# Kernel optimization log

Measured on AMD Instinct MI355X. Metric: run time of the kernel, lower is better.

The kernel has to match this reference:

```python
import jax, jax.numpy as jnp
import numpy as np
from itertools import permutations

B, Nm, S, K, H, OUT = 32, 128, 16, 4, 128, 1
LG, LI, LGL = 3, 2, 2  # num_layer, num_layer_id, num_layer_global
EPS = 1e-5


def _ln(x, g, b):
    m = jnp.mean(x, -1, keepdims=True)
    v = jnp.mean(jnp.square(x - m), -1, keepdims=True)
    return (x - m) * jax.lax.rsqrt(v + EPS) * g + b


def _block(x, W1, b1, W2, b2, g, bn):
    # Linear -> ReLU -> Linear -> LayerNorm -> ReLU
    h = jax.nn.relu(x @ W1 + b1)
    return jax.nn.relu(_ln(h @ W2 + b2, g, bn))


def setup_inputs() -> dict:
    key = jax.random.key(0)
    ks = iter(jax.random.split(key, 64))
    nrm = lambda shape, s=0.05: jax.random.normal(next(ks), shape, jnp.float32) * s
    x = nrm((B, Nm, 1), 1.0)
    adj = (jax.random.uniform(next(ks), (B, Nm, Nm)) < 0.05).astype(jnp.float32)
    # allperm: all permutations of [1..K-1] with 0 prepended, transposed -> (K, permdim)
    ap = np.array(list(permutations(range(1, K))), dtype=np.int32)
    ap = np.concatenate([np.zeros((ap.shape[0], 1), np.int32), ap], axis=1).T
    allperm = jnp.asarray(ap)
    Ssub = B * S
    base = jax.random.randint(next(ks), (Ssub,), 0, Nm - K)
    subgs = base[:, None] + jnp.arange(K, dtype=jnp.int32)[None, :]  # distinct nodes per subgraph
    num_subg = jnp.full((B,), S, jnp.int32)
    num_node = jnp.full((B,), Nm, jnp.int32)
    d = dict(x=x, adj=adj,
             idemb=nrm((K + 2, H)),
             in_W1=nrm((1, H)), in_b1=jnp.zeros((H,)), in_W2=nrm((H, H)), in_b2=jnp.zeros((H,)),
             in_g=jnp.ones((H,)), in_bn=jnp.zeros((H,)),
             gW1=nrm((LG, H, H)), gb1=jnp.zeros((LG, H)), gW2=nrm((LG, H, H)), gb2=jnp.zeros((LG, H)),
             gg=jnp.ones((LG, H)), gbn=jnp.zeros((LG, H)),
             iW1=nrm((LI, H, H)), ib1=jnp.zeros((LI, H)), iW2=nrm((LI, H, H)), ib2=jnp.zeros((LI, H)),
             ig=jnp.ones((LI, H)), ibn=jnp.zeros((LI, H)),
             glW1=nrm((LGL, H, H)), glb1=jnp.zeros((LGL, H)), glW2=nrm((LGL, H, H)), glb2=jnp.zeros((LGL, H)),
             glg=jnp.ones((LGL, H)), glbn=jnp.zeros((LGL, H)),
             s1_W=nrm((H, H)), s1_b=jnp.zeros((H,)), s2_W=nrm((H, H)), s2_b=jnp.zeros((H,)),
             rW1=nrm((H, H)), rb1=jnp.zeros((H,)), rW2=nrm((H, H)), rb2=jnp.zeros((H,)),
             rg=jnp.ones((H,)), rbn=jnp.zeros((H,)),
             out_W=nrm((H, OUT)), out_b=jnp.zeros((OUT,)),
             subgs=subgs, num_subg=num_subg, num_node=num_node, allperm=allperm)
    return d


def reference(x, adj, idemb, in_W1, in_b1, in_W2, in_b2, in_g, in_bn,
              gW1, gb1, gW2, gb2, gg, gbn,
              iW1, ib1, iW2, ib2, ig, ibn,
              glW1, glb1, glW2, glb2, glg, glbn,
              s1_W, s1_b, s2_W, s2_b,
              rW1, rb1, rW2, rb2, rg, rbn,
              out_W, out_b, subgs, num_subg, num_node, allperm):
    Bsz, N = x.shape[0], x.shape[1]
    Ssub, k = subgs.shape
    permdim = allperm.shape[1]
    # input embedding MLP
    h = _block(x, in_W1, in_b1, in_W2, in_b2, in_g, in_bn)  # (B, Nm, H)
    Hd = h.shape[-1]
    # subgraph -> graph batch map (ns_b = S per graph; Ssub static)
    subgbatch = jnp.repeat(jnp.arange(Bsz), num_subg, total_repeat_length=Ssub)
    # identity labeling: z starts as ones, labeled nodes get idemb(allperm[pos])
    lb = jnp.repeat(jnp.arange(Ssub), k)          # label batch (subgraph idx)
    lnodes = subgs.reshape(-1)                    # node ids within graph
    ni = jnp.tile(jnp.arange(k), Ssub)            # position within subgraph
    vals = idemb[allperm[ni]]                     # (Ssub*k, permdim, H)
    z = jnp.ones((Ssub, N, permdim, Hd), x.dtype)
    z = z.at[lb, lnodes].multiply(vals)
    # graph message passing on full graphs
    for l in range(gW1.shape[0]):
        m = jnp.einsum('bij,bjd->bid', adj, h)
        h = h + _block(m, gW1[l], gb1[l], gW2[l], gb2[l], gg[l], gbn[l])
    hs = h[subgbatch]        # (Ssub, Nm, H)
    sadj = adj[subgbatch]    # (Ssub, Nm, Nm)
    # id message passing over permutation channels
    for l in range(iW1.shape[0]):
        m = jnp.einsum('bij,bjpd->bipd', sadj, z)
        z = z + _block(m, iW1[l], ib1[l], iW2[l], ib2[l], ig[l], ibn[l])
    # zero out padded (null) nodes
    null_mask = jnp.arange(N)[None, :] >= num_node[:, None]  # (B, Nm)
    z = jnp.where(null_mask[subgbatch][:, :, None, None], 0.0, z)
    z = jax.nn.relu(z.mean(axis=2) @ s1_W + s1_b)  # setmlp1, (Ssub, Nm, H)
    hs = hs + z
    for l in range(glW1.shape[0]):
        m = jnp.einsum('bij,bjd->bid', sadj, hs)
        hs = hs + _block(m, glW1[l], glb1[l], glW2[l], glb2[l], glg[l], glbn[l])
    hs = jax.nn.relu(hs.sum(axis=1) @ s2_W + s2_b)  # setmlp2, (Ssub, H)
    pooled = jax.ops.segment_max(hs, subgbatch, num_segments=Bsz)  # global max pool
    pooled = pooled + _block(pooled, rW1, rb1, rW2, rb2, rg, rbn)  # setmlp3 (1 layer)
    return pooled @ out_W + out_b  # (B, OUT)
```

## Files before the change

kernel.cpp:

```cpp
#include <hip/hip_runtime.h>
#include <hip/hip_bf16.h>
#include <string.h>

typedef __hip_bfloat16 bf16;
typedef short v8s __attribute__((ext_vector_type(8)));
typedef float v4f __attribute__((ext_vector_type(4)));

#define H_ 128
#define P_ 6
#define K_ 4

__device__ __forceinline__ float ldf(const float* p, size_t i) { return p[i]; }
__device__ __forceinline__ float ldf(const bf16* p, size_t i) { return __bfloat162float(p[i]); }

__device__ __forceinline__ float s2f(short s) {
    unsigned int u = ((unsigned int)(unsigned short)s) << 16;
    float f; __builtin_memcpy(&f, &u, 4); return f;
}
__device__ __forceinline__ short f2s(float v) {
    bf16 h = __float2bfloat16(v);
    short s; __builtin_memcpy(&s, &h, 2); return s;
}
__device__ __forceinline__ v4f MFMA(v8s a, v8s b, v4f c) {
    return __builtin_amdgcn_mfma_f32_16x16x32_bf16(a, b, c, 0, 0, 0);
}

__global__ __launch_bounds__(128) void k_deg(const float* __restrict__ adj, float* __restrict__ degf)
{
    __shared__ float red[128];
    const int row = blockIdx.x, t = threadIdx.x;
    red[t] = adj[(size_t)row * 128 + t];
    __syncthreads();
    for (int s = 64; s > 0; s >>= 1) {
        if (t < s) red[t] += red[t + s];
        __syncthreads();
    }
    if (t == 0) degf[row] = red[0];
}

__global__ __launch_bounds__(128) void k_adjb(const float* __restrict__ adj, bf16* __restrict__ adjb)
{
    const size_t i = (size_t)blockIdx.x * 128 + threadIdx.x;
    adjb[i] = __float2bfloat16(adj[i]);
}

__global__ __launch_bounds__(128) void k_wt8(
    const float* s0, const float* s1, const float* s2, const float* s3,
    const float* s4, const float* s5, const float* s6, const float* s7,
    bf16* __restrict__ dst)
{
    const int w = blockIdx.x >> 7, n = blockIdx.x & 127, k = threadIdx.x;
    const float* arr[8] = {s0, s1, s2, s3, s4, s5, s6, s7};
    dst[(size_t)w * 16384 + n * 128 + k] = __float2bfloat16(arr[w][k * 128 + n]);
}

__global__ __launch_bounds__(128) void k_wt1(const float* __restrict__ src, bf16* __restrict__ dst)
{
    const int n = blockIdx.x, k = threadIdx.x;
    dst[n * 128 + k] = __float2bfloat16(src[k * 128 + n]);
}

template<bool DO_MM1, bool HAS_RES>
__global__ __launch_bounds__(128) void k_block(
    const float* __restrict__ in, const float* __restrict__ res, float* __restrict__ out,
    const float* __restrict__ W1, const float* __restrict__ b1,
    const float* __restrict__ W2, const float* __restrict__ b2,
    const float* __restrict__ gam, const float* __restrict__ bet)
{
    __shared__ float sA[16][136];
    __shared__ float sB[16][136];
    __shared__ float sStat[32];
    const int hd = threadIdx.x;
    const size_t row0 = (size_t)blockIdx.x * 16;
    #pragma unroll
    for (int r = 0; r < 16; ++r) sA[r][hd] = in[(row0 + r) * H_ + hd];
    __syncthreads();
    float acc[16];
    if (DO_MM1) {
        #pragma unroll
        for (int r = 0; r < 16; ++r) acc[r] = b1[hd];
        for (int k = 0; k < H_; k += 4) {
            float w0 = W1[(k+0)*H_+hd], w1 = W1[(k+1)*H_+hd], w2 = W1[(k+2)*H_+hd], w3 = W1[(k+3)*H_+hd];
            #pragma unroll
            for (int r = 0; r < 16; ++r) {
                float4 a = *(const float4*)&sA[r][k];
                acc[r] = fmaf(a.x, w0, acc[r]); acc[r] = fmaf(a.y, w1, acc[r]);
                acc[r] = fmaf(a.z, w2, acc[r]); acc[r] = fmaf(a.w, w3, acc[r]);
            }
        }
        #pragma unroll
        for (int r = 0; r < 16; ++r) sB[r][hd] = fmaxf(acc[r], 0.f);
    } else {
        #pragma unroll
        for (int r = 0; r < 16; ++r) sB[r][hd] = sA[r][hd];
    }
    __syncthreads();
    #pragma unroll
    for (int r = 0; r < 16; ++r) acc[r] = b2[hd];
    for (int k = 0; k < H_; k += 4) {
        float w0 = W2[(k+0)*H_+hd], w1 = W2[(k+1)*H_+hd], w2 = W2[(k+2)*H_+hd], w3 = W2[(k+3)*H_+hd];
        #pragma unroll
        for (int r = 0; r < 16; ++r) {
            float4 a = *(const float4*)&sB[r][k];
            acc[r] = fmaf(a.x, w0, acc[r]); acc[r] = fmaf(a.y, w1, acc[r]);
            acc[r] = fmaf(a.z, w2, acc[r]); acc[r] = fmaf(a.w, w3, acc[r]);
        }
    }
    __syncthreads();
    #pragma unroll
    for (int r = 0; r < 16; ++r) sA[r][hd] = acc[r];
    __syncthreads();
    if (hd < 16) {
        float s = 0.f, ss = 0.f;
        for (int k = 0; k < H_; ++k) { float v = sA[hd][k]; s += v; ss += v * v; }
        float mean = s * (1.f / H_);
        float var = ss * (1.f / H_) - mean * mean;
        sStat[hd] = mean; sStat[16 + hd] = rsqrtf(var + 1e-5f);
    }
    __syncthreads();
    float gv = gam[hd], bv = bet[hd];
    #pragma unroll
    for (int r = 0; r < 16; ++r) {
        float v = fmaxf((acc[r] - sStat[r]) * sStat[16 + r] * gv + bv, 0.f);
        if (HAS_RES) v += res[(row0 + r) * H_ + hd];
        out[(row0 + r) * H_ + hd] = v;
    }
}

template<bool GATHER, typename T>
__global__ __launch_bounds__(128) void k_gemm_relu(
    const T* __restrict__ in, const float* __restrict__ res, float* __restrict__ out,
    const float* __restrict__ W, const float* __restrict__ b)
{
    __shared__ float sA[16][136];
    const int hd = threadIdx.x;
    const size_t row0 = (size_t)blockIdx.x * 16;
    #pragma unroll
    for (int r = 0; r < 16; ++r) sA[r][hd] = ldf(in, (row0 + r) * H_ + hd);
    __syncthreads();
    float acc[16];
    #pragma unroll
    for (int r = 0; r < 16; ++r) acc[r] = b[hd];
    for (int k = 0; k < H_; k += 4) {
        float w0 = W[(k+0)*H_+hd], w1 = W[(k+1)*H_+hd], w2 = W[(k+2)*H_+hd], w3 = W[(k+3)*H_+hd];
        #pragma unroll
        for (int r = 0; r < 16; ++r) {
            float4 a = *(const float4*)&sA[r][k];
            acc[r] = fmaf(a.x, w0, acc[r]); acc[r] = fmaf(a.y, w1, acc[r]);
            acc[r] = fmaf(a.z, w2, acc[r]); acc[r] = fmaf(a.w, w3, acc[r]);
        }
    }
    #pragma unroll
    for (int r = 0; r < 16; ++r) {
        size_t rr = row0 + r;
        float v = fmaxf(acc[r], 0.f);
        if (GATHER) {
            int i = (int)(rr & 127);
            int g = (int)(rr >> 11);
            v += res[((size_t)(g * 128 + i)) * H_ + hd];
        }
        out[rr * H_ + hd] = v;
    }
}

__global__ __launch_bounds__(256) void k_h_fused(
    const float* __restrict__ x, const bf16* __restrict__ adjb,
    const float* __restrict__ inW1, const float* __restrict__ inb1,
    const bf16* __restrict__ inW2t, const float* __restrict__ inb2,
    const float* __restrict__ ing, const float* __restrict__ inbn,
    const bf16* __restrict__ WTg,
    const float* __restrict__ gb1, const float* __restrict__ gb2,
    const float* __restrict__ gg, const float* __restrict__ gbn,
    float* __restrict__ hb)
{
    __shared__ __align__(16) short sHsT[128][136];
    __shared__ __align__(16) short sM[128][136];
    __shared__ float sP[15][128];
    const int t = threadIdx.x;
    const int g = blockIdx.x;
    const int wave = t >> 6, lane = t & 63, quad = lane >> 4, l16 = lane & 15;
    const int wrow = wave << 5;

    for (int u = t; u < 15 * 128; u += 256) {
        const int a = u >> 7, n = u & 127;
        const float* src;
        if (a == 0) src = inb2;
        else if (a == 1) src = ing;
        else if (a == 2) src = inbn;
        else {
            const int l = (a - 3) >> 2, pp = (a - 3) & 3;
            src = (pp == 0) ? gb1 + l * 128 : (pp == 1) ? gb2 + l * 128
                : (pp == 2) ? gg + l * 128 : gbn + l * 128;
        }
        sP[a][n] = src[n];
    }

    v8s aA[2][4];
    {
        const bf16* ar = adjb + (size_t)g * 16384;
        #pragma unroll
        for (int mt = 0; mt < 2; ++mt)
            #pragma unroll
            for (int kk = 0; kk < 4; ++kk)
                aA[mt][kk] = *(const v8s*)(ar + (size_t)(wrow + mt * 16 + l16) * 128 + kk * 32 + quad * 8);
    }

    {
        const int i = t >> 1, half = (t & 1) * 64;
        const float xv = x[(size_t)g * 128 + i];
        #pragma unroll
        for (int fb = 0; fb < 64; fb += 8) {
            v8s pk;
            #pragma unroll
            for (int e = 0; e < 8; ++e)
                pk[e] = f2s(fmaxf(fmaf(xv, inW1[half + fb + e], inb1[half + fb + e]), 0.f));
            *(v8s*)&sM[i][half + fb] = pk;
        }
    }
    __syncthreads();

    v4f acc[2][8];
    #pragma unroll
    for (int mt = 0; mt < 2; ++mt)
        #pragma unroll
        for (int nt = 0; nt < 8; ++nt) acc[mt][nt] = (v4f){0.f, 0.f, 0.f, 0.f};
    #pragma unroll
    for (int kk = 0; kk < 4; ++kk) {
        v8s a0 = *(const v8s*)&sM[wrow + l16][kk * 32 + quad * 8];
        v8s a1 = *(const v8s*)&sM[wrow + 16 + l16][kk * 32 + quad * 8];
        #pragma unroll
        for (int nt = 0; nt < 8; ++nt) {
            v8s b = *(const v8s*)(inW2t + (nt * 16 + l16) * 128 + kk * 32 + quad * 8);
            acc[0][nt] = MFMA(a0, b, acc[0][nt]);
            acc[1][nt] = MFMA(a1, b, acc[1][nt]);
        }
    }
    float hs_reg[2][8][4];
    #pragma unroll
    for (int mt = 0; mt < 2; ++mt)
        #pragma unroll
        for (int r = 0; r < 4; ++r) {
            float s = 0.f, qq = 0.f;
            #pragma unroll
            for (int nt = 0; nt < 8; ++nt) {
                float u = acc[mt][nt][r] + sP[0][nt * 16 + l16];
                acc[mt][nt][r] = u;
                s += u; qq += u * u;
            }
            #pragma unroll
            for (int d = 1; d < 16; d <<= 1) {
                s += __shfl_xor(s, d);
                qq += __shfl_xor(qq, d);
            }
            float mn = s * (1.f / 128.f);
            float rs = rsqrtf(qq * (1.f / 128.f) - mn * mn + 1e-5f);
            const int i = wrow + mt * 16 + quad * 4 + r;
            #pragma unroll
            for (int nt = 0; nt < 8; ++nt) {
                const int n = nt * 16 + l16;
                float v = fmaxf((acc[mt][nt][r] - mn) * rs * sP[1][n] + sP[2][n], 0.f);
                hs_reg[mt][nt][r] = v;
                sHsT[n][i] = f2s(v);
            }
        }
    __syncthreads();

    for (int l = 0; l < 3; ++l) {
        const bf16* W1t = WTg + (size_t)(2 * l) * 16384;
        const bf16* W2t = WTg + (size_t)(2 * l + 1) * 16384;
        #pragma unroll
        for (int mt = 0; mt < 2; ++mt)
            #pragma unroll
            for (int nt = 0; nt < 8; ++nt) acc[mt][nt] = (v4f){0.f, 0.f, 0.f, 0.f};
        #pragma unroll
        for (int kk = 0; kk < 4; ++kk)
            #pragma unroll
            for (int nt = 0; nt < 8; ++nt) {
                v8s b = *(const v8s*)&sHsT[nt * 16 + l16][kk * 32 + quad * 8];
                acc[0][nt] = MFMA(aA[0][kk], b, acc[0][nt]);
                acc[1][nt] = MFMA(aA[1][kk], b, acc[1][nt]);
            }
        #pragma unroll
        for (int nt = 0; nt < 8; ++nt)
            #pragma unroll
            for (int mt = 0; mt < 2; ++mt)
                #pragma unroll
                for (int r = 0; r < 4; ++r)
                    sM[wrow + mt * 16 + quad * 4 + r][nt * 16 + l16] = f2s(acc[mt][nt][r]);
        __syncthreads();
        #pragma unroll
        for (int mt = 0; mt < 2; ++mt)
            #pragma unroll
            for (int nt = 0; nt < 8; ++nt) acc[mt][nt] = (v4f){0.f, 0.f, 0.f, 0.f};
        #pragma unroll
        for (int kk = 0; kk < 4; ++kk) {
            v8s a0 = *(const v8s*)&sM[wrow + l16][kk * 32 + quad * 8];
            v8s a1 = *(const v8s*)&sM[wrow + 16 + l16][kk * 32 + quad * 8];
            #pragma unroll
            for (int nt = 0; nt < 8; ++nt) {
                v8s b = *(const v8s*)(W1t + (nt * 16 + l16) * 128 + kk * 32 + quad * 8);
                acc[0][nt] = MFMA(a0, b, acc[0][nt]);
                acc[1][nt] = MFMA(a1, b, acc[1][nt]);
            }
        }
        #pragma unroll
        for (int nt = 0; nt < 8; ++nt) {
            float bb = sP[3 + 4 * l + 0][nt * 16 + l16];
            #pragma unroll
            for (int mt = 0; mt < 2; ++mt)
                #pragma unroll
                for (int r = 0; r < 4; ++r)
                    sM[wrow + mt * 16 + quad * 4 + r][nt * 16 + l16] = f2s(fmaxf(acc[mt][nt][r] + bb, 0.f));
        }
        #pragma unroll
        for (int mt = 0; mt < 2; ++mt)
            #pragma unroll
            for (int nt = 0; nt < 8; ++nt) acc[mt][nt] = (v4f){0.f, 0.f, 0.f, 0.f};
        #pragma unroll
        for (int kk = 0; kk < 4; ++kk) {
            v8s a0 = *(const v8s*)&sM[wrow + l16][kk * 32 + quad * 8];
            v8s a1 = *(const v8s*)&sM[wrow + 16 + l16][kk * 32 + quad * 8];
            #pragma unroll
            for (int nt = 0; nt < 8; ++nt) {
                v8s b = *(const v8s*)(W2t + (nt * 16 + l16) * 128 + kk * 32 + quad * 8);
                acc[0][nt] = MFMA(a0, b, acc[0][nt]);
                acc[1][nt] = MFMA(a1, b, acc[1][nt]);
            }
        }
        #pragma unroll
        for (int mt = 0; mt < 2; ++mt)
            #pragma unroll
            for (int r = 0; r < 4; ++r) {
                float s = 0.f, qq = 0.f;
                #pragma unroll
                for (int nt = 0; nt < 8; ++nt) {
                    float u = acc[mt][nt][r] + sP[3 + 4 * l + 1][nt * 16 + l16];
                    acc[mt][nt][r] = u;
                    s += u; qq += u * u;
                }
                #pragma unroll
                for (int d = 1; d < 16; d <<= 1) {
                    s += __shfl_xor(s, d);
                    qq += __shfl_xor(qq, d);
                }
                float mn = s * (1.f / 128.f);
                float rs = rsqrtf(qq * (1.f / 128.f) - mn * mn + 1e-5f);
                const int i = wrow + mt * 16 + quad * 4 + r;
                #pragma unroll
                for (int nt = 0; nt < 8; ++nt) {
                    const int n = nt * 16 + l16;
                    float v = fmaxf((acc[mt][nt][r] - mn) * rs * sP[3 + 4 * l + 2][n] + sP[3 + 4 * l + 3][n], 0.f);
                    float h2 = hs_reg[mt][nt][r] + v;
                    hs_reg[mt][nt][r] = h2;
                    sHsT[n][i] = f2s(h2);
                }
            }
        __syncthreads();
    }

    #pragma unroll
    for (int mt = 0; mt < 2; ++mt)
        #pragma unroll
        for (int nt = 0; nt < 8; ++nt)
            #pragma unroll
            for (int r = 0; r < 4; ++r) {
                const int i = wrow + mt * 16 + quad * 4 + r;
                const int n = nt * 16 + l16;
                hb[((size_t)(g * 128 + i)) * 128 + n] = hs_reg[mt][nt][r];
            }
}

__global__ __launch_bounds__(256) void k_id1_fused(
    const float* __restrict__ adj, const float* __restrict__ degf,
    const int* __restrict__ subgs, const int* __restrict__ allperm,
    const float* __restrict__ idemb, bf16* __restrict__ outb,
    const bf16* __restrict__ W1t, const float* __restrict__ b1,
    const bf16* __restrict__ W2t, const float* __restrict__ b2,
    const float* __restrict__ gam, const float* __restrict__ bet)
{
    __shared__ __align__(16) short sB[128][136];
    __shared__ float sE[K_][128];
    const int t = threadIdx.x;
    const int bi = blockIdx.x;
    const int b_s = bi / 6, p = bi - b_s * 6;
    const int g = b_s >> 4;
    const int wave = t >> 6, lane = t & 63;
    const int quad = lane >> 4, l16 = lane & 15;
    const int wrow = wave << 5;

    int nodeq[K_];
    #pragma unroll
    for (int q = 0; q < K_; ++q) nodeq[q] = subgs[b_s * K_ + q];

    for (int u = t; u < K_ * 128; u += 256) {
        const int q = u >> 7, f = u & 127;
        sE[q][f] = idemb[(size_t)allperm[q * P_ + p] * H_ + f] - 1.f;
    }
    __syncthreads();

    {
        const int i = t >> 1, half = (t & 1) * 64;
        const int gi = g * 128 + i;
        const float dg = degf[gi];
        float aq[K_];
        #pragma unroll
        for (int q = 0; q < K_; ++q) aq[q] = adj[(size_t)gi * 128 + nodeq[q]];
        #pragma unroll
        for (int f = 0; f < 64; ++f) {
            float v = dg;
            #pragma unroll
            for (int q = 0; q < K_; ++q) v = fmaf(aq[q], sE[q][half + f], v);
            sB[i][half + f] = f2s(v);
        }
    }
    __syncthreads();

    v4f acc[2][8];
    #pragma unroll
    for (int mt = 0; mt < 2; ++mt)
        #pragma unroll
        for (int nt = 0; nt < 8; ++nt) acc[mt][nt] = (v4f){0.f, 0.f, 0.f, 0.f};
    #pragma unroll
    for (int kk = 0; kk < 4; ++kk) {
        v8s a0 = *(const v8s*)&sB[wrow + l16][kk * 32 + quad * 8];
        v8s a1 = *(const v8s*)&sB[wrow + 16 + l16][kk * 32 + quad * 8];
        #pragma unroll
        for (int nt = 0; nt < 8; ++nt) {
            v8s b = *(const v8s*)(W1t + (nt * 16 + l16) * 128 + kk * 32 + quad * 8);
            acc[0][nt] = MFMA(a0, b, acc[0][nt]);
            acc[1][nt] = MFMA(a1, b, acc[1][nt]);
        }
    }
    #pragma unroll
    for (int nt = 0; nt < 8; ++nt) {
        float bb = b1[nt * 16 + l16];
        #pragma unroll
        for (int mt = 0; mt < 2; ++mt)
            #pragma unroll
            for (int r = 0; r < 4; ++r)
                sB[wrow + mt * 16 + quad * 4 + r][nt * 16 + l16] = f2s(fmaxf(acc[mt][nt][r] + bb, 0.f));
    }
    #pragma unroll
    for (int mt = 0; mt < 2; ++mt)
        #pragma unroll
        for (int nt = 0; nt < 8; ++nt) acc[mt][nt] = (v4f){0.f, 0.f, 0.f, 0.f};
    #pragma unroll
    for (int kk = 0; kk < 4; ++kk) {
        v8s a0 = *(const v8s*)&sB[wrow + l16][kk * 32 + quad * 8];
        v8s a1 = *(const v8s*)&sB[wrow + 16 + l16][kk * 32 + quad * 8];
        #pragma unroll
        for (int nt = 0; nt < 8; ++nt) {
            v8s b = *(const v8s*)(W2t + (nt * 16 + l16) * 128 + kk * 32 + quad * 8);
            acc[0][nt] = MFMA(a0, b, acc[0][nt]);
            acc[1][nt] = MFMA(a1, b, acc[1][nt]);
        }
    }
    float bb2[8], gv[8], bv[8];
    #pragma unroll
    for (int nt = 0; nt < 8; ++nt) {
        int n = nt * 16 + l16;
        bb2[nt] = b2[n]; gv[nt] = gam[n]; bv[nt] = bet[n];
    }
    #pragma unroll
    for (int mt = 0; mt < 2; ++mt)
        #pragma unroll
        for (int r = 0; r < 4; ++r) {
            float s = 0.f, q = 0.f;
            #pragma unroll
            for (int nt = 0; nt < 8; ++nt) {
                float u = acc[mt][nt][r] + bb2[nt];
                acc[mt][nt][r] = u;
                s += u; q += u * u;
            }
            #pragma unroll
            for (int d = 1; d < 16; d <<= 1) {
                s += __shfl_xor(s, d);
                q += __shfl_xor(q, d);
            }
            float mn = s * (1.f / 128.f);
            float rs = rsqrtf(q * (1.f / 128.f) - mn * mn + 1e-5f);
            #pragma unroll
            for (int nt = 0; nt < 8; ++nt) {
                float v = fmaxf((acc[mt][nt][r] - mn) * rs * gv[nt] + bv[nt], 0.f);
                sB[wrow + mt * 16 + quad * 4 + r][nt * 16 + l16] = f2s(v + 1.0f);
            }
        }
    __syncthreads();
    {
        const int f = t >> 1, nh = (t & 1) * 64;
        const short* flat = &sB[0][0];
        bf16* dst = outb + (size_t)bi * 16384 + (size_t)f * 128 + nh;
        #pragma unroll
        for (int u = 0; u < 8; ++u) {
            v8s pk;
            #pragma unroll
            for (int e = 0; e < 8; ++e) pk[e] = flat[(nh + u * 8 + e) * 136 + f];
            *(v8s*)(dst + u * 8) = pk;
        }
    }
}

__global__ __launch_bounds__(256) void k_id2_v9(
    const bf16* __restrict__ z2t, bf16* __restrict__ zm,
    const bf16* __restrict__ adjb, const int* __restrict__ num_node,
    const int* __restrict__ subgs, const int* __restrict__ allperm,
    const float* __restrict__ idemb,
    const bf16* __restrict__ W1t, const float* __restrict__ b1,
    const bf16* __restrict__ W2t, const float* __restrict__ b2,
    const float* __restrict__ gam, const float* __restrict__ bet)
{
    __shared__ __align__(16) short sB[128][136];
    __shared__ float sP[4][128];
    const int t = threadIdx.x;
    const int b_s = blockIdx.x;
    const int g = b_s >> 4;
    const int wave = t >> 6, lane = t & 63, quad = lane >> 4, l16 = lane & 15;
    const int wrow = wave << 5;

    #pragma unroll
    for (int u = 0; u < 2; ++u) {
        const int v = t + u * 256;
        const int a = v >> 7, n = v & 127;
        const float* src = (a == 0) ? b1 : (a == 1) ? b2 : (a == 2) ? gam : bet;
        sP[a][n] = src[n];
    }

    v8s aA[2][4];
    {
        const bf16* ar = adjb + (size_t)g * 16384;
        #pragma unroll
        for (int mt = 0; mt < 2; ++mt)
            #pragma unroll
            for (int kk = 0; kk < 4; ++kk)
                aA[mt][kk] = *(const v8s*)(ar + (size_t)(wrow + mt * 16 + l16) * 128 + kk * 32 + quad * 8);
    }
    int nodeq[K_];
    #pragma unroll
    for (int q = 0; q < K_; ++q) nodeq[q] = subgs[b_s * K_ + q];

    float macc[2][8][4];
    #pragma unroll
    for (int mt = 0; mt < 2; ++mt)
        #pragma unroll
        for (int nt = 0; nt < 8; ++nt)
            #pragma unroll
            for (int r = 0; r < 4; ++r) macc[mt][nt][r] = 0.f;

    const int sf = t >> 1, shalf = (t & 1) * 64;

    for (int p = 0; p < P_; ++p) {
        {
            const bf16* src = z2t + ((size_t)(b_s * P_ + p)) * 16384 + (size_t)sf * 128 + shalf;
            #pragma unroll
            for (int u = 0; u < 8; ++u)
                *(v8s*)&sB[sf][shalf + u * 8] = *(const v8s*)(src + u * 8);
        }
        __syncthreads();
        if (t < 128) {
            #pragma unroll
            for (int q = 0; q < K_; ++q) {
                float e = idemb[(size_t)allperm[q * P_ + p] * H_ + t] - 1.f;
                short* cell = &sB[t][nodeq[q]];
                *cell = f2s(s2f(*cell) + e);
            }
        }
        __syncthreads();
        #pragma unroll
        for (int mt = 0; mt < 2; ++mt)
            #pragma unroll
            for (int nt = 0; nt < 8; ++nt) {
                const int n = nt * 16 + l16;
                #pragma unroll
                for (int r = 0; r < 4; ++r)
                    macc[mt][nt][r] += s2f(sB[n][wrow + mt * 16 + quad * 4 + r]);
            }
        v4f acc[2][8];
        #pragma unroll
        for (int mt = 0; mt < 2; ++mt)
            #pragma unroll
            for (int nt = 0; nt < 8; ++nt) acc[mt][nt] = (v4f){0.f, 0.f, 0.f, 0.f};
        #pragma unroll
        for (int kk = 0; kk < 4; ++kk)
            #pragma unroll
            for (int nt = 0; nt < 8; ++nt) {
                v8s b = *(const v8s*)&sB[nt * 16 + l16][kk * 32 + quad * 8];
                acc[0][nt] = MFMA(aA[0][kk], b, acc[0][nt]);
                acc[1][nt] = MFMA(aA[1][kk], b, acc[1][nt]);
            }
        __syncthreads();
        #pragma unroll
        for (int nt = 0; nt < 8; ++nt)
            #pragma unroll
            for (int mt = 0; mt < 2; ++mt)
                #pragma unroll
                for (int r = 0; r < 4; ++r)
                    sB[wrow + mt * 16 + quad * 4 + r][nt * 16 + l16] = f2s(acc[mt][nt][r]);
        #pragma unroll
        for (int mt = 0; mt < 2; ++mt)
            #pragma unroll
            for (int nt = 0; nt < 8; ++nt) acc[mt][nt] = (v4f){0.f, 0.f, 0.f, 0.f};
        #pragma unroll
        for (int kk = 0; kk < 4; ++kk) {
            v8s a0 = *(const v8s*)&sB[wrow + l16][kk * 32 + quad * 8];
            v8s a1 = *(const v8s*)&sB[wrow + 16 + l16][kk * 32 + quad * 8];
            #pragma unroll
            for (int nt = 0; nt < 8; ++nt) {
                v8s b = *(const v8s*)(W1t + (nt * 16 + l16) * 128 + kk * 32 + quad * 8);
                acc[0][nt] = MFMA(a0, b, acc[0][nt]);
                acc[1][nt] = MFMA(a1, b, acc[1][nt]);
            }
        }
        #pragma unroll
        for (int nt = 0; nt < 8; ++nt) {
            float bb = sP[0][nt * 16 + l16];
            #pragma unroll
            for (int mt = 0; mt < 2; ++mt)
                #pragma unroll
                for (int r = 0; r < 4; ++r)
                    sB[wrow + mt * 16 + quad * 4 + r][nt * 16 + l16] = f2s(fmaxf(acc[mt][nt][r] + bb, 0.f));
        }
        #pragma unroll
        for (int mt = 0; mt < 2; ++mt)
            #pragma unroll
            for (int nt = 0; nt < 8; ++nt) acc[mt][nt] = (v4f){0.f, 0.f, 0.f, 0.f};
        #pragma unroll
        for (int kk = 0; kk < 4; ++kk) {
            v8s a0 = *(const v8s*)&sB[wrow + l16][kk * 32 + quad * 8];
            v8s a1 = *(const v8s*)&sB[wrow + 16 + l16][kk * 32 + quad * 8];
            #pragma unroll
            for (int nt = 0; nt < 8; ++nt) {
                v8s b = *(const v8s*)(W2t + (nt * 16 + l16) * 128 + kk * 32 + quad * 8);
                acc[0][nt] = MFMA(a0, b, acc[0][nt]);
                acc[1][nt] = MFMA(a1, b, acc[1][nt]);
            }
        }
        #pragma unroll
        for (int mt = 0; mt < 2; ++mt)
            #pragma unroll
            for (int r = 0; r < 4; ++r) {
                float s = 0.f, qq = 0.f;
                #pragma unroll
                for (int nt = 0; nt < 8; ++nt) {
                    float u = acc[mt][nt][r] + sP[1][nt * 16 + l16];
                    acc[mt][nt][r] = u;
                    s += u; qq += u * u;
                }
                #pragma unroll
                for (int d = 1; d < 16; d <<= 1) {
                    s += __shfl_xor(s, d);
                    qq += __shfl_xor(qq, d);
                }
                float mn = s * (1.f / 128.f);
                float rs = rsqrtf(qq * (1.f / 128.f) - mn * mn + 1e-5f);
                #pragma unroll
                for (int nt = 0; nt < 8; ++nt) {
                    const int n = nt * 16 + l16;
                    macc[mt][nt][r] += fmaxf((acc[mt][nt][r] - mn) * rs * sP[2][n] + sP[3][n], 0.f);
                }
            }
        __syncthreads();
    }
    const int nn = num_node[g];
    #pragma unroll
    for (int mt = 0; mt < 2; ++mt)
        #pragma unroll
        for (int nt = 0; nt < 8; ++nt)
            #pragma unroll
            for (int r = 0; r < 4; ++r) {
                const int i = wrow + mt * 16 + quad * 4 + r;
                const int n = nt * 16 + l16;
                float v = (i >= nn) ? 0.f : macc[mt][nt][r] * (1.f / 6.f);
                zm[((size_t)(b_s * 128 + i)) * 128 + n] = __float2bfloat16(v);
            }
}

__global__ __launch_bounds__(256) void k_gl_fused(
    const bf16* __restrict__ zm, const float* __restrict__ hb,
    const bf16* __restrict__ adjb,
    const bf16* __restrict__ s1Wt, const float* __restrict__ s1_b,
    const bf16* __restrict__ WTgl,
    const float* __restrict__ glb1, const float* __restrict__ glb2,
    const float* __restrict__ glg, const float* __restrict__ glbn,
    float* __restrict__ hsum)
{
    __shared__ __align__(16) short sHsT[128][136];
    __shared__ __align__(16) short sM[128][136];
    __shared__ float sP[9][128];
    const int t = threadIdx.x;
    const int b_s = blockIdx.x;
    const int g = b_s >> 4;
    const int wave = t >> 6, lane = t & 63, quad = lane >> 4, l16 = lane & 15;
    const int wrow = wave << 5;

    for (int u = t; u < 9 * 128; u += 256) {
        const int a = u >> 7, n = u & 127;
        const float* src =
            (a == 0) ? glb1 : (a == 1) ? glb2 : (a == 2) ? glg : (a == 3) ? glbn :
            (a == 4) ? glb1 + 128 : (a == 5) ? glb2 + 128 : (a == 6) ? glg + 128 :
            (a == 7) ? glbn + 128 : s1_b;
        sP[a][n] = src[n];
    }

    v8s aA[2][4];
    {
        const bf16* ar = adjb + (size_t)g * 16384;
        #pragma unroll
        for (int mt = 0; mt < 2; ++mt)
            #pragma unroll
            for (int kk = 0; kk < 4; ++kk)
                aA[mt][kk] = *(const v8s*)(ar + (size_t)(wrow + mt * 16 + l16) * 128 + kk * 32 + quad * 8);
    }

    v4f acc[2][8];
    #pragma unroll
    for (int mt = 0; mt < 2; ++mt)
        #pragma unroll
        for (int nt = 0; nt < 8; ++nt) acc[mt][nt] = (v4f){0.f, 0.f, 0.f, 0.f};
    #pragma unroll
    for (int kk = 0; kk < 4; ++kk) {
        v8s a0 = *(const v8s*)(zm + ((size_t)(b_s * 128) + wrow + l16) * 128 + kk * 32 + quad * 8);
        v8s a1 = *(const v8s*)(zm + ((size_t)(b_s * 128) + wrow + 16 + l16) * 128 + kk * 32 + quad * 8);
        #pragma unroll
        for (int nt = 0; nt < 8; ++nt) {
            v8s b = *(const v8s*)(s1Wt + (nt * 16 + l16) * 128 + kk * 32 + quad * 8);
            acc[0][nt] = MFMA(a0, b, acc[0][nt]);
            acc[1][nt] = MFMA(a1, b, acc[1][nt]);
        }
    }
    __syncthreads();
    float hs_reg[2][8][4];
    #pragma unroll
    for (int mt = 0; mt < 2; ++mt)
        #pragma unroll
        for (int nt = 0; nt < 8; ++nt)
            #pragma unroll
            for (int r = 0; r < 4; ++r) {
                const int i = wrow + mt * 16 + quad * 4 + r;
                const int n = nt * 16 + l16;
                float v = fmaxf(acc[mt][nt][r] + sP[8][n], 0.f);
                v += hb[((size_t)(g * 128 + i)) * 128 + n];
                hs_reg[mt][nt][r] = v;
                sHsT[n][i] = f2s(v);
            }
    __syncthreads();

    for (int l = 0; l < 2; ++l) {
        const bf16* W1t = WTgl + (size_t)(2 * l) * 16384;
        const bf16* W2t = WTgl + (size_t)(2 * l + 1) * 16384;
        #pragma unroll
        for (int mt = 0; mt < 2; ++mt)
            #pragma unroll
            for (int nt = 0; nt < 8; ++nt) acc[mt][nt] = (v4f){0.f, 0.f, 0.f, 0.f};
        #pragma unroll
        for (int kk = 0; kk < 4; ++kk)
            #pragma unroll
            for (int nt = 0; nt < 8; ++nt) {
                v8s b = *(const v8s*)&sHsT[nt * 16 + l16][kk * 32 + quad * 8];
                acc[0][nt] = MFMA(aA[0][kk], b, acc[0][nt]);
                acc[1][nt] = MFMA(aA[1][kk], b, acc[1][nt]);
            }
        #pragma unroll
        for (int nt = 0; nt < 8; ++nt)
            #pragma unroll
            for (int mt = 0; mt < 2; ++mt)
                #pragma unroll
                for (int r = 0; r < 4; ++r)
                    sM[wrow + mt * 16 + quad * 4 + r][nt * 16 + l16] = f2s(acc[mt][nt][r]);
        __syncthreads();
        #pragma unroll
        for (int mt = 0; mt < 2; ++mt)
            #pragma unroll
            for (int nt = 0; nt < 8; ++nt) acc[mt][nt] = (v4f){0.f, 0.f, 0.f, 0.f};
        #pragma unroll
        for (int kk = 0; kk < 4; ++kk) {
            v8s a0 = *(const v8s*)&sM[wrow + l16][kk * 32 + quad * 8];
            v8s a1 = *(const v8s*)&sM[wrow + 16 + l16][kk * 32 + quad * 8];
            #pragma unroll
            for (int nt = 0; nt < 8; ++nt) {
                v8s b = *(const v8s*)(W1t + (nt * 16 + l16) * 128 + kk * 32 + quad * 8);
                acc[0][nt] = MFMA(a0, b, acc[0][nt]);
                acc[1][nt] = MFMA(a1, b, acc[1][nt]);
            }
        }
        #pragma unroll
        for (int nt = 0; nt < 8; ++nt) {
            float bb = sP[4 * l + 0][nt * 16 + l16];
            #pragma unroll
            for (int mt = 0; mt < 2; ++mt)
                #pragma unroll
                for (int r = 0; r < 4; ++r)
                    sM[wrow + mt * 16 + quad * 4 + r][nt * 16 + l16] = f2s(fmaxf(acc[mt][nt][r] + bb, 0.f));
        }
        #pragma unroll
        for (int mt = 0; mt < 2; ++mt)
            #pragma unroll
            for (int nt = 0; nt < 8; ++nt) acc[mt][nt] = (v4f){0.f, 0.f, 0.f, 0.f};
        #pragma unroll
        for (int kk = 0; kk < 4; ++kk) {
            v8s a0 = *(const v8s*)&sM[wrow + l16][kk * 32 + quad * 8];
            v8s a1 = *(const v8s*)&sM[wrow + 16 + l16][kk * 32 + quad * 8];
            #pragma unroll
            for (int nt = 0; nt < 8; ++nt) {
                v8s b = *(const v8s*)(W2t + (nt * 16 + l16) * 128 + kk * 32 + quad * 8);
                acc[0][nt] = MFMA(a0, b, acc[0][nt]);
                acc[1][nt] = MFMA(a1, b, acc[1][nt]);
            }
        }
        #pragma unroll
        for (int mt = 0; mt < 2; ++mt)
            #pragma unroll
            for (int r = 0; r < 4; ++r) {
                float s = 0.f, qq = 0.f;
                #pragma unroll
                for (int nt = 0; nt < 8; ++nt) {
                    float u = acc[mt][nt][r] + sP[4 * l + 1][nt * 16 + l16];
                    acc[mt][nt][r] = u;
                    s += u; qq += u * u;
                }
                #pragma unroll
                for (int d = 1; d < 16; d <<= 1) {
                    s += __shfl_xor(s, d);
                    qq += __shfl_xor(qq, d);
                }
                float mn = s * (1.f / 128.f);
                float rs = rsqrtf(qq * (1.f / 128.f) - mn * mn + 1e-5f);
                const int i = wrow + mt * 16 + quad * 4 + r;
                #pragma unroll
                for (int nt = 0; nt < 8; ++nt) {
                    const int n = nt * 16 + l16;
                    float v = fmaxf((acc[mt][nt][r] - mn) * rs * sP[4 * l + 2][n] + sP[4 * l + 3][n], 0.f);
                    float h2 = hs_reg[mt][nt][r] + v;
                    hs_reg[mt][nt][r] = h2;
                    sHsT[n][i] = f2s(h2);
                }
            }
        __syncthreads();
    }

    float* sRedf = (float*)&sM[0][0];
    #pragma unroll
    for (int nt = 0; nt < 8; ++nt) {
        float part = 0.f;
        #pragma unroll
        for (int mt = 0; mt < 2; ++mt)
            #pragma unroll
            for (int r = 0; r < 4; ++r) part += hs_reg[mt][nt][r];
        sRedf[(wave * 4 + quad) * 128 + nt * 16 + l16] = part;
    }
    __syncthreads();
    if (t < 128) {
        float s = 0.f;
        #pragma unroll
        for (int r = 0; r < 16; ++r) s += sRedf[r * 128 + t];
        hsum[(size_t)b_s * 128 + t] = s;
    }
}

__global__ __launch_bounds__(128) void k_maxpool(const float* __restrict__ hs2, float* __restrict__ pooled)
{
    const int g = blockIdx.x, hd = threadIdx.x;
    float m = -INFINITY;
    for (int s = 0; s < 16; ++s) m = fmaxf(m, hs2[((size_t)(g * 16 + s)) * H_ + hd]);
    pooled[(size_t)g * H_ + hd] = m;
}

__global__ __launch_bounds__(128) void k_out(const float* __restrict__ pooled2,
    const float* __restrict__ out_W, const float* __restrict__ out_b, float* __restrict__ out)
{
    __shared__ float red[128];
    const int g = blockIdx.x, hd = threadIdx.x;
    red[hd] = pooled2[(size_t)g * H_ + hd] * out_W[hd];
    __syncthreads();
    for (int s = 64; s > 0; s >>= 1) {
        if (hd < s) red[hd] += red[hd + s];
        __syncthreads();
    }
    if (hd == 0) out[g] = red[0] + out_b[0];
}

extern "C" void kernel_launch(void* const* d_in, const int* in_sizes, int n_in,
                              void* d_out, int out_size, void* d_ws, size_t ws_size,
                              hipStream_t stream)
{
    (void)in_sizes; (void)n_in; (void)out_size; (void)ws_size;
    const float* x     = (const float*)d_in[0];
    const float* adj   = (const float*)d_in[1];
    const float* idemb = (const float*)d_in[2];
    const float* in_W1 = (const float*)d_in[3];
    const float* in_b1 = (const float*)d_in[4];
    const float* in_W2 = (const float*)d_in[5];
    const float* in_b2 = (const float*)d_in[6];
    const float* in_g  = (const float*)d_in[7];
    const float* in_bn = (const float*)d_in[8];
    const float* gW1   = (const float*)d_in[9];
    const float* gb1   = (const float*)d_in[10];
    const float* gW2   = (const float*)d_in[11];
    const float* gb2   = (const float*)d_in[12];
    const float* gg    = (const float*)d_in[13];
    const float* gbn   = (const float*)d_in[14];
    const float* iW1   = (const float*)d_in[15];
    const float* ib1   = (const float*)d_in[16];
    const float* iW2   = (const float*)d_in[17];
    const float* ib2   = (const float*)d_in[18];
    const float* ig    = (const float*)d_in[19];
    const float* ibn   = (const float*)d_in[20];
    const float* glW1  = (const float*)d_in[21];
    const float* glb1  = (const float*)d_in[22];
    const float* glW2  = (const float*)d_in[23];
    const float* glb2  = (const float*)d_in[24];
    const float* glg   = (const float*)d_in[25];
    const float* glbn  = (const float*)d_in[26];
    const float* s1_W  = (const float*)d_in[27];
    const float* s1_b  = (const float*)d_in[28];
    const float* s2_W  = (const float*)d_in[29];
    const float* s2_b  = (const float*)d_in[30];
    const float* rW1   = (const float*)d_in[31];
    const float* rb1   = (const float*)d_in[32];
    const float* rW2   = (const float*)d_in[33];
    const float* rb2   = (const float*)d_in[34];
    const float* rg    = (const float*)d_in[35];
    const float* rbn   = (const float*)d_in[36];
    const float* out_W = (const float*)d_in[37];
    const float* out_b = (const float*)d_in[38];
    const int* subgs   = (const int*)d_in[39];
    const int* num_node= (const int*)d_in[41];
    const int* allperm = (const int*)d_in[42];

    const size_t MB_ = (size_t)512 * 128 * P_ * H_ * 2;
    char* w = (char*)d_ws;
    bf16*  mz     = (bf16*)(w);
    bf16*  s1Wt   = (bf16*)(w + 33554432ull);
    bf16*  zm     = (bf16*)(w + MB_);
    bf16*  WT     = (bf16*)(w + MB_ + 16777216ull);
    char*  wc     = w + MB_ + 16777216ull + 262144ull;
    float* hb     = (float*)(wc);
    bf16*  adjb   = (bf16*)(wc + 2097152ull);
    bf16*  WT2    = (bf16*)(wc + 3145728ull);
    float* hsum   = (float*)(wc + 4194304ull);
    float* hs2    = (float*)(wc + 4456448ull);
    float* pooled = (float*)(wc + 4718592ull);
    float* pooled2= (float*)(wc + 4734976ull);
    float* degf   = (float*)(wc + 4964352ull);
    float* outp   = (float*)d_out;

    k_deg<<<4096, 128, 0, stream>>>(adj, degf);
    k_wt8<<<1024, 128, 0, stream>>>(iW1, iW2, iW1 + 16384, iW2 + 16384,
                                    glW1, glW2, glW1 + 16384, glW2 + 16384, WT);
    k_wt8<<<1024, 128, 0, stream>>>(in_W2, gW1, gW2, gW1 + 16384,
                                    gW2 + 16384, gW1 + 32768, gW2 + 32768, in_W2, WT2);
    k_adjb<<<4096, 128, 0, stream>>>(adj, adjb);

    k_h_fused<<<32, 256, 0, stream>>>(x, adjb, in_W1, in_b1,
        WT2, in_b2, in_g, in_bn,
        WT2 + 16384, gb1, gb2, gg, gbn, hb);

    k_id1_fused<<<3072, 256, 0, stream>>>(adj, degf, subgs, allperm, idemb, mz,
        WT, ib1, WT + 16384, ib2, ig, ibn);

    k_id2_v9<<<512, 256, 0, stream>>>(mz, zm, adjb, num_node, subgs, allperm, idemb,
        WT + 2 * 16384, ib1 + 128, WT + 3 * 16384, ib2 + 128, ig + 128, ibn + 128);

    k_wt1<<<128, 128, 0, stream>>>(s1_W, s1Wt);

    k_gl_fused<<<512, 256, 0, stream>>>(zm, hb, adjb, s1Wt, s1_b,
        WT + 4 * 16384, glb1, glb2, glg, glbn, hsum);

    k_gemm_relu<false, float><<<32, 128, 0, stream>>>(hsum, nullptr, hs2, s2_W, s2_b);
    k_maxpool<<<32, 128, 0, stream>>>(hs2, pooled);
    k_block<true, true><<<2, 128, 0, stream>>>(pooled, pooled, pooled2,
        rW1, rb1, rW2, rb2, rg, rbn);
    k_out<<<32, 128, 0, stream>>>(pooled2, out_W, out_b, outp);
}
```

Before: 589.8 us.

## Fuse tail kernels into one and share a single LDS buffer in gl kernel

Replaces the separate s2 gemm, max-pool, readout block and output-dot kernels with a single per-graph tail kernel, removing three launches and intermediate global buffers. In the gl fused kernel, the transposed-hs and message LDS buffers are merged into one, with extra barriers added so the buffer can be safely reused. This roughly halves LDS use, which can allow more resident blocks, at the cost of extra synchronisation.

```diff
diff --git a/kernel.cpp b/kernel.cpp
--- a/kernel.cpp
+++ b/kernel.cpp
@@ -9,9 +9,6 @@
 #define H_ 128
 #define P_ 6
 #define K_ 4
-
-__device__ __forceinline__ float ldf(const float* p, size_t i) { return p[i]; }
-__device__ __forceinline__ float ldf(const bf16* p, size_t i) { return __bfloat162float(p[i]); }
 
 __device__ __forceinline__ float s2f(short s) {
     unsigned int u = ((unsigned int)(unsigned short)s) << 16;
@@ -58,109 +55,6 @@
 {
     const int n = blockIdx.x, k = threadIdx.x;
     dst[n * 128 + k] = __float2bfloat16(src[k * 128 + n]);
-}
-
-template<bool DO_MM1, bool HAS_RES>
-__global__ __launch_bounds__(128) void k_block(
-    const float* __restrict__ in, const float* __restrict__ res, float* __restrict__ out,
-    const float* __restrict__ W1, const float* __restrict__ b1,
-    const float* __restrict__ W2, const float* __restrict__ b2,
-    const float* __restrict__ gam, const float* __restrict__ bet)
-{
-    __shared__ float sA[16][136];
-    __shared__ float sB[16][136];
-    __shared__ float sStat[32];
-    const int hd = threadIdx.x;
-    const size_t row0 = (size_t)blockIdx.x * 16;
-    #pragma unroll
-    for (int r = 0; r < 16; ++r) sA[r][hd] = in[(row0 + r) * H_ + hd];
-    __syncthreads();
-    float acc[16];
-    if (DO_MM1) {
-        #pragma unroll
-        for (int r = 0; r < 16; ++r) acc[r] = b1[hd];
-        for (int k = 0; k < H_; k += 4) {
-            float w0 = W1[(k+0)*H_+hd], w1 = W1[(k+1)*H_+hd], w2 = W1[(k+2)*H_+hd], w3 = W1[(k+3)*H_+hd];
-            #pragma unroll
-            for (int r = 0; r < 16; ++r) {
-                float4 a = *(const float4*)&sA[r][k];
-                acc[r] = fmaf(a.x, w0, acc[r]); acc[r] = fmaf(a.y, w1, acc[r]);
-                acc[r] = fmaf(a.z, w2, acc[r]); acc[r] = fmaf(a.w, w3, acc[r]);
-            }
-        }
-        #pragma unroll
-        for (int r = 0; r < 16; ++r) sB[r][hd] = fmaxf(acc[r], 0.f);
-    } else {
-        #pragma unroll
-        for (int r = 0; r < 16; ++r) sB[r][hd] = sA[r][hd];
-    }
-    __syncthreads();
-    #pragma unroll
-    for (int r = 0; r < 16; ++r) acc[r] = b2[hd];
-    for (int k = 0; k < H_; k += 4) {
-        float w0 = W2[(k+0)*H_+hd], w1 = W2[(k+1)*H_+hd], w2 = W2[(k+2)*H_+hd], w3 = W2[(k+3)*H_+hd];
-        #pragma unroll
-        for (int r = 0; r < 16; ++r) {
-            float4 a = *(const float4*)&sB[r][k];
-            acc[r] = fmaf(a.x, w0, acc[r]); acc[r] = fmaf(a.y, w1, acc[r]);
-            acc[r] = fmaf(a.z, w2, acc[r]); acc[r] = fmaf(a.w, w3, acc[r]);
-        }
-    }
-    __syncthreads();
-    #pragma unroll
-    for (int r = 0; r < 16; ++r) sA[r][hd] = acc[r];
-    __syncthreads();
-    if (hd < 16) {
-        float s = 0.f, ss = 0.f;
-        for (int k = 0; k < H_; ++k) { float v = sA[hd][k]; s += v; ss += v * v; }
-        float mean = s * (1.f / H_);
-        float var = ss * (1.f / H_) - mean * mean;
-        sStat[hd] = mean; sStat[16 + hd] = rsqrtf(var + 1e-5f);
-    }
-    __syncthreads();
-    float gv = gam[hd], bv = bet[hd];
-    #pragma unroll
-    for (int r = 0; r < 16; ++r) {
-        float v = fmaxf((acc[r] - sStat[r]) * sStat[16 + r] * gv + bv, 0.f);
-        if (HAS_RES) v += res[(row0 + r) * H_ + hd];
-        out[(row0 + r) * H_ + hd] = v;
-    }
-}
-
-template<bool GATHER, typename T>
-__global__ __launch_bounds__(128) void k_gemm_relu(
-    const T* __restrict__ in, const float* __restrict__ res, float* __restrict__ out,
-    const float* __restrict__ W, const float* __restrict__ b)
-{
-    __shared__ float sA[16][136];
-    const int hd = threadIdx.x;
-    const size_t row0 = (size_t)blockIdx.x * 16;
-    #pragma unroll
-    for (int r = 0; r < 16; ++r) sA[r][hd] = ldf(in, (row0 + r) * H_ + hd);
-    __syncthreads();
-    float acc[16];
-    #pragma unroll
-    for (int r = 0; r < 16; ++r) acc[r] = b[hd];
-    for (int k = 0; k < H_; k += 4) {
-        float w0 = W[(k+0)*H_+hd], w1 = W[(k+1)*H_+hd], w2 = W[(k+2)*H_+hd], w3 = W[(k+3)*H_+hd];
-        #pragma unroll
-        for (int r = 0; r < 16; ++r) {
-            float4 a = *(const float4*)&sA[r][k];
-            acc[r] = fmaf(a.x, w0, acc[r]); acc[r] = fmaf(a.y, w1, acc[r]);
-            acc[r] = fmaf(a.z, w2, acc[r]); acc[r] = fmaf(a.w, w3, acc[r]);
-        }
-    }
-    #pragma unroll
-    for (int r = 0; r < 16; ++r) {
-        size_t rr = row0 + r;
-        float v = fmaxf(acc[r], 0.f);
-        if (GATHER) {
-            int i = (int)(rr & 127);
-            int g = (int)(rr >> 11);
-            v += res[((size_t)(g * 128 + i)) * H_ + hd];
-        }
-        out[rr * H_ + hd] = v;
-    }
 }
 
 __global__ __launch_bounds__(256) void k_h_fused(
@@ -683,8 +577,7 @@
     const float* __restrict__ glg, const float* __restrict__ glbn,
     float* __restrict__ hsum)
 {
-    __shared__ __align__(16) short sHsT[128][136];
-    __shared__ __align__(16) short sM[128][136];
+    __shared__ __align__(16) short sB[128][136];
     __shared__ float sP[9][128];
     const int t = threadIdx.x;
     const int b_s = blockIdx.x;
@@ -740,7 +633,7 @@
                 float v = fmaxf(acc[mt][nt][r] + sP[8][n], 0.f);
                 v += hb[((size_t)(g * 128 + i)) * 128 + n];
                 hs_reg[mt][nt][r] = v;
-                sHsT[n][i] = f2s(v);
+                sB[n][i] = f2s(v);
             }
     __syncthreads();
 
@@ -755,26 +648,26 @@
         for (int kk = 0; kk < 4; ++kk)
             #pragma unroll
             for (int nt = 0; nt < 8; ++nt) {
-                v8s b = *(const v8s*)&sHsT[nt * 16 + l16][kk * 32 + quad * 8];
+                v8s b = *(const v8s*)&sB[nt * 16 + l16][kk * 32 + quad * 8];
                 acc[0][nt] = MFMA(aA[0][kk], b, acc[0][nt]);
                 acc[1][nt] = MFMA(aA[1][kk], b, acc[1][nt]);
             }
+        __syncthreads();
         #pragma unroll
         for (int nt = 0; nt < 8; ++nt)
             #pragma unroll
             for (int mt = 0; mt < 2; ++mt)
                 #pragma unroll
                 for (int r = 0; r < 4; ++r)
-                    sM[wrow + mt * 16 + quad * 4 + r][nt * 16 + l16] = f2s(acc[mt][nt][r]);
-        __syncthreads();
+                    sB[wrow + mt * 16 + quad * 4 + r][nt * 16 + l16] = f2s(acc[mt][nt][r]);
         #pragma unroll
         for (int mt = 0; mt < 2; ++mt)
             #pragma unroll
             for (int nt = 0; nt < 8; ++nt) acc[mt][nt] = (v4f){0.f, 0.f, 0.f, 0.f};
         #pragma unroll
         for (int kk = 0; kk < 4; ++kk) {
-            v8s a0 = *(const v8s*)&sM[wrow + l16][kk * 32 + quad * 8];
-            v8s a1 = *(const v8s*)&sM[wrow + 16 + l16][kk * 32 + quad * 8];
+            v8s a0 = *(const v8s*)&sB[wrow + l16][kk * 32 + quad * 8];
+            v8s a1 = *(const v8s*)&sB[wrow + 16 + l16][kk * 32 + quad * 8];
             #pragma unroll
             for (int nt = 0; nt < 8; ++nt) {
                 v8s b = *(const v8s*)(W1t + (nt * 16 + l16) * 128 + kk * 32 + quad * 8);
@@ -789,7 +682,7 @@
             for (int mt = 0; mt < 2; ++mt)
                 #pragma unroll
                 for (int r = 0; r < 4; ++r)
-                    sM[wrow + mt * 16 + quad * 4 + r][nt * 16 + l16] = f2s(fmaxf(acc[mt][nt][r] + bb, 0.f));
+                    sB[wrow + mt * 16 + quad * 4 + r][nt * 16 + l16] = f2s(fmaxf(acc[mt][nt][r] + bb, 0.f));
         }
         #pragma unroll
         for (int mt = 0; mt < 2; ++mt)
@@ -797,8 +690,8 @@
             for (int nt = 0; nt < 8; ++nt) acc[mt][nt] = (v4f){0.f, 0.f, 0.f, 0.f};
         #pragma unroll
         for (int kk = 0; kk < 4; ++kk) {
-            v8s a0 = *(const v8s*)&sM[wrow + l16][kk * 32 + quad * 8];
-            v8s a1 = *(const v8s*)&sM[wrow + 16 + l16][kk * 32 + quad * 8];
+            v8s a0 = *(const v8s*)&sB[wrow + l16][kk * 32 + quad * 8];
+            v8s a1 = *(const v8s*)&sB[wrow + 16 + l16][kk * 32 + quad * 8];
             #pragma unroll
             for (int nt = 0; nt < 8; ++nt) {
                 v8s b = *(const v8s*)(W2t + (nt * 16 + l16) * 128 + kk * 32 + quad * 8);
@@ -806,6 +699,7 @@
                 acc[1][nt] = MFMA(a1, b, acc[1][nt]);
             }
         }
+        __syncthreads();
         #pragma unroll
         for (int mt = 0; mt < 2; ++mt)
             #pragma unroll
@@ -831,13 +725,13 @@
                     float v = fmaxf((acc[mt][nt][r] - mn) * rs * sP[4 * l + 2][n] + sP[4 * l + 3][n], 0.f);
                     float h2 = hs_reg[mt][nt][r] + v;
                     hs_reg[mt][nt][r] = h2;
-                    sHsT[n][i] = f2s(h2);
+                    sB[n][i] = f2s(h2);
                 }
             }
         __syncthreads();
     }
 
-    float* sRedf = (float*)&sM[0][0];
+    float* sRedf = (float*)&sB[0][0];
     #pragma unroll
     for (int nt = 0; nt < 8; ++nt) {
         float part = 0.f;
@@ -856,26 +750,66 @@
     }
 }
 
-__global__ __launch_bounds__(128) void k_maxpool(const float* __restrict__ hs2, float* __restrict__ pooled)
+__global__ __launch_bounds__(128) void k_tail(const float* __restrict__ hsum,
+    const float* __restrict__ s2W, const float* __restrict__ s2b,
+    const float* __restrict__ rW1, const float* __restrict__ rb1,
+    const float* __restrict__ rW2, const float* __restrict__ rb2,
+    const float* __restrict__ rg, const float* __restrict__ rbn,
+    const float* __restrict__ outW, const float* __restrict__ outb,
+    float* __restrict__ out)
 {
-    const int g = blockIdx.x, hd = threadIdx.x;
-    float m = -INFINITY;
-    for (int s = 0; s < 16; ++s) m = fmaxf(m, hs2[((size_t)(g * 16 + s)) * H_ + hd]);
-    pooled[(size_t)g * H_ + hd] = m;
-}
-
-__global__ __launch_bounds__(128) void k_out(const float* __restrict__ pooled2,
-    const float* __restrict__ out_W, const float* __restrict__ out_b, float* __restrict__ out)
-{
+    __shared__ float sA[16][136];
+    __shared__ float sV[128];
     __shared__ float red[128];
     const int g = blockIdx.x, hd = threadIdx.x;
-    red[hd] = pooled2[(size_t)g * H_ + hd] * out_W[hd];
+    #pragma unroll
+    for (int r = 0; r < 16; ++r) sA[r][hd] = hsum[((size_t)(g * 16 + r)) * 128 + hd];
+    __syncthreads();
+    float acc[16];
+    #pragma unroll
+    for (int r = 0; r < 16; ++r) acc[r] = s2b[hd];
+    for (int k = 0; k < 128; k += 4) {
+        float w0 = s2W[(k+0)*128+hd], w1 = s2W[(k+1)*128+hd], w2 = s2W[(k+2)*128+hd], w3 = s2W[(k+3)*128+hd];
+        #pragma unroll
+        for (int r = 0; r < 16; ++r) {
+            float4 a = *(const float4*)&sA[r][k];
+            acc[r] = fmaf(a.x, w0, acc[r]); acc[r] = fmaf(a.y, w1, acc[r]);
+            acc[r] = fmaf(a.z, w2, acc[r]); acc[r] = fmaf(a.w, w3, acc[r]);
+        }
+    }
+    float pool = 0.f;
+    pool = -INFINITY;
+    #pragma unroll
+    for (int r = 0; r < 16; ++r) pool = fmaxf(pool, fmaxf(acc[r], 0.f));
+    sV[hd] = pool;
+    __syncthreads();
+    float t1 = rb1[hd];
+    for (int k = 0; k < 128; ++k) t1 = fmaf(sV[k], rW1[k * 128 + hd], t1);
+    t1 = fmaxf(t1, 0.f);
+    red[hd] = t1;
+    __syncthreads();
+    float u = rb2[hd];
+    for (int k = 0; k < 128; ++k) u = fmaf(red[k], rW2[k * 128 + hd], u);
+    float* rs1 = (float*)&sA[0][0];
+    float* rs2 = (float*)&sA[2][0];
+    rs1[hd] = u; rs2[hd] = u * u;
+    __syncthreads();
+    for (int s = 64; s > 0; s >>= 1) {
+        if (hd < s) { rs1[hd] += rs1[hd + s]; rs2[hd] += rs2[hd + s]; }
+        __syncthreads();
+    }
+    float mn = rs1[0] * (1.f / 128.f);
+    float var = rs2[0] * (1.f / 128.f) - mn * mn;
+    float rstd = rsqrtf(var + 1e-5f);
+    float p2 = fmaxf((u - mn) * rstd * rg[hd] + rbn[hd], 0.f) + sV[hd];
+    __syncthreads();
+    red[hd] = p2 * outW[hd];
     __syncthreads();
     for (int s = 64; s > 0; s >>= 1) {
         if (hd < s) red[hd] += red[hd + s];
         __syncthreads();
     }
-    if (hd == 0) out[g] = red[0] + out_b[0];
+    if (hd == 0) out[g] = red[0] + outb[0];
 }
 
 extern "C" void kernel_launch(void* const* d_in, const int* in_sizes, int n_in,
@@ -937,9 +871,6 @@
     bf16*  adjb   = (bf16*)(wc + 2097152ull);
     bf16*  WT2    = (bf16*)(wc + 3145728ull);
     float* hsum   = (float*)(wc + 4194304ull);
-    float* hs2    = (float*)(wc + 4456448ull);
-    float* pooled = (float*)(wc + 4718592ull);
-    float* pooled2= (float*)(wc + 4734976ull);
     float* degf   = (float*)(wc + 4964352ull);
     float* outp   = (float*)d_out;
 
@@ -965,9 +896,6 @@
     k_gl_fused<<<512, 256, 0, stream>>>(zm, hb, adjb, s1Wt, s1_b,
         WT + 4 * 16384, glb1, glb2, glg, glbn, hsum);
 
-    k_gemm_relu<false, float><<<32, 128, 0, stream>>>(hsum, nullptr, hs2, s2_W, s2_b);
-    k_maxpool<<<32, 128, 0, stream>>>(hs2, pooled);
-    k_block<true, true><<<2, 128, 0, stream>>>(pooled, pooled, pooled2,
-        rW1, rb1, rW2, rb2, rg, rbn);
-    k_out<<<32, 128, 0, stream>>>(pooled2, out_W, out_b, outp);
-}
+    k_tail<<<32, 128, 0, stream>>>(hsum, s2_W, s2_b, rW1, rb1, rW2, rb2,
+        rg, rbn, out_W, out_b, outp);
+}
```

After: 564.9 us. 1.04x faster.
